# Optimization experiments

Measured on AMD Instinct MI355X. Metric: run time of the kernel, lower is better.

## Reference

```python
import jax, jax.numpy as jnp
import numpy as np

DECAY = 0.99
EPS = 1e-05
B, T, DIM, N_EMBED = 64, 1024, 256, 1024


def setup_inputs() -> dict:
    key = jax.random.key(0)
    k1, k2 = jax.random.split(key, 2)
    input_ = jax.random.normal(k1, (B, T, DIM), dtype=jnp.float32)
    embed = jax.random.normal(k2, (DIM, N_EMBED), dtype=jnp.float32)  # buffer 'embed'
    cluster_size = jnp.zeros((N_EMBED,), dtype=jnp.float32)           # buffer 'cluster_size'
    embed_avg = embed.copy()                                          # buffer 'embed_avg'
    return {"input_": input_, "embed": embed, "cluster_size": cluster_size, "embed_avg": embed_avg}


def reference(input_, embed, cluster_size, embed_avg):
    n_embed = embed.shape[1]
    flatten = input_.reshape(-1, embed.shape[0])  # [N, dim]
    dist = (jnp.sum(flatten * flatten, axis=-1, keepdims=True)
            - 2.0 * flatten @ embed
            + jnp.sum(embed * embed, axis=0, keepdims=True))
    embed_ind = jnp.argmin(dist, axis=1)  # (-dist).max(1) == argmin(dist)
    quantize = jnp.take(embed.T, embed_ind, axis=0).reshape(input_.shape)

    # training-mode EMA codebook update (buffers are detached in torch)
    # embed_onehot_sum = onehot.sum(0); embed_sum = flatten.T @ onehot
    # implemented via segment_sum (same math, no NxK one-hot materialized)
    ones = jnp.ones((flatten.shape[0],), dtype=flatten.dtype)
    embed_onehot_sum = jax.ops.segment_sum(ones, embed_ind, num_segments=n_embed)
    embed_sum = jax.ops.segment_sum(flatten, embed_ind, num_segments=n_embed).T  # [dim, n_embed]

    new_cluster_size = cluster_size * DECAY + (1.0 - DECAY) * embed_onehot_sum
    # NOTE: original code applies .mul_(decay) TWICE to embed_avg -> decay**2 (faithful)
    new_embed_avg = embed_avg * (DECAY * DECAY) + (1.0 - DECAY) * embed_sum
    n = jnp.sum(new_cluster_size)
    cs = (new_cluster_size + EPS) / (n + n_embed * EPS) * n
    new_embed = new_embed_avg / cs[None, :]

    diff = jnp.mean((jax.lax.stop_gradient(quantize) - input_) ** 2)
    quantize_st = input_ + jax.lax.stop_gradient(quantize - input_)
    return quantize_st, diff, embed_ind, new_cluster_size, new_embed_avg, new_embed
```

## Files before the change

kernel.cpp:

```cpp
#include <hip/hip_runtime.h>
#include <float.h>

#define DECAY 0.99f
#define EPS 1e-5f
#define NROWS 65536
#define DIM 256
#define NEMB 1024
#define CH 64
#define MAXSUB 2048

#define GLOBAL_AS __attribute__((address_space(1)))
#define LOCAL_AS  __attribute__((address_space(3)))

typedef _Float16 f16;
typedef _Float16 half8 __attribute__((ext_vector_type(8)));
typedef float f32x4 __attribute__((ext_vector_type(4)));

__global__ __launch_bounds__(256) void k_enorm(const float* __restrict__ embed,
                                               float* __restrict__ enorm2,
                                               int* __restrict__ counts) {
    int kk = threadIdx.x & 63;
    int dg = threadIdx.x >> 6;
    int k  = blockIdx.x * 64 + kk;
    float s = 0.f;
    for (int d = dg; d < DIM; d += 4) {
        float v = embed[(size_t)d * NEMB + k];
        s = fmaf(v, v, s);
    }
    __shared__ float red[4][64];
    red[dg][kk] = s;
    __syncthreads();
    if (dg == 0) enorm2[k] = red[0][kk] + red[1][kk] + red[2][kk] + red[3][kk];
    int gt = blockIdx.x * 256 + threadIdx.x;
    if (gt < NEMB) counts[gt] = 0;
}

__global__ __launch_bounds__(256) void k_prep(const float* __restrict__ embed,
                                              float* __restrict__ embedT,
                                              f16* __restrict__ ehlT) {
    __shared__ float tile[32][33];
    int c0 = blockIdx.x * 32, d0 = blockIdx.y * 32;
    int tx = threadIdx.x, ty = threadIdx.y;
#pragma unroll
    for (int i = 0; i < 4; i++)
        tile[ty + 8 * i][tx] = embed[(size_t)(d0 + ty + 8 * i) * NEMB + c0 + tx];
    __syncthreads();
#pragma unroll
    for (int i = 0; i < 4; i++) {
        int c = c0 + ty + 8 * i;
        int d = d0 + tx;
        float v = tile[tx][ty + 8 * i];
        embedT[(size_t)c * DIM + d] = v;
        f16 h = (f16)v;
        ehlT[(size_t)c * 512 + d]       = h;
        ehlT[(size_t)c * 512 + 256 + d] = (f16)(v - (float)h);
    }
}

#define LDS_A  0
#define LDS_B0 131072
#define LDS_B1 147456
#define LDS_SZ 163840

__global__ __launch_bounds__(512, 2) void k_argmin_mfma(const float* __restrict__ input,
                                                        const f16* __restrict__ ehlT,
                                                        const float* __restrict__ enorm2,
                                                        int* __restrict__ ind,
                                                        float* __restrict__ out_ind,
                                                        int* __restrict__ counts) {
    __shared__ char lds[LDS_SZ];
    const int tid  = threadIdx.x;
    const int lane = tid & 63;
    const int w    = tid >> 6;
    const int wr   = w >> 2;
    const int wc   = w & 3;
    const int rb   = blockIdx.x * 128;
    const int l15  = lane & 15;
    const int lkh  = lane >> 4;
    const int swa  = (l15 & 7) << 4;
    const int swb  = ((l15 >> 1) & 3) << 4;
    const int slot_log   = (lane & 3) ^ ((lane >> 3) & 3);
    const int gl_laneoff = (lane >> 2) * 512 + slot_log * 8;

    float e2a[4][4];
#pragma unroll
    for (int s = 0; s < 4; ++s)
#pragma unroll
        for (int fc = 0; fc < 4; ++fc)
            e2a[s][fc] = enorm2[s * 256 + wc * 64 + fc * 16 + l15];

#pragma unroll
    for (int i = 0; i < 2; i++) {
        int chunkid = w * 2 + i;
        const f16* src = ehlT + (size_t)chunkid * 8192 + gl_laneoff;
        __builtin_amdgcn_global_load_lds((const GLOBAL_AS unsigned*)src,
            (LOCAL_AS unsigned*)(lds + LDS_B0 + chunkid * 1024), 16, 0, 0);
    }

#pragma unroll
    for (int it8 = 0; it8 < 4; it8++) {
        int task = tid + 512 * it8;
        int row = task >> 4, ch = task & 15;
        const float4* g = (const float4*)(input + (size_t)(rb + row) * DIM + ch * 16);
        float fv[16];
        *(float4*)(fv + 0)  = g[0];
        *(float4*)(fv + 4)  = g[1];
        *(float4*)(fv + 8)  = g[2];
        *(float4*)(fv + 12) = g[3];
        half8 hh[2], llv[2];
#pragma unroll
        for (int u = 0; u < 2; u++)
#pragma unroll
            for (int e = 0; e < 8; e++) {
                float x = fv[u * 8 + e];
                f16 h = (f16)x;
                hh[u][e]  = h;
                llv[u][e] = (f16)(x - (float)h);
            }
        int rbase = row * 1024;
        int sw = (row & 7) << 4;
        *(half8*)(lds + LDS_A + rbase + (((ch * 2    ) * 16) ^ sw)) = hh[0];
        *(half8*)(lds + LDS_A + rbase + (((ch * 2 + 1) * 16) ^ sw)) = hh[1];
        *(half8*)(lds + LDS_A + rbase + (((32 + ch * 2) * 16) ^ sw)) = llv[0];
        *(half8*)(lds + LDS_A + rbase + (((33 + ch * 2) * 16) ^ sw)) = llv[1];
    }
    __syncthreads();

    float bv[16];
    int   bi[16];
#pragma unroll
    for (int q = 0; q < 16; q++) { bv[q] = FLT_MAX; bi[q] = 0x7fffffff; }

    int p = 0;
    for (int ct = 0; ct < 4; ct++) {
        const int cb = ct * 256;
        f32x4 acc[4][4];
#pragma unroll
        for (int fr = 0; fr < 4; fr++)
#pragma unroll
            for (int fc = 0; fc < 4; fc++) acc[fr][fc] = (f32x4){0.f, 0.f, 0.f, 0.f};

        for (int kt = 0; kt < 24; kt++) {
            const int it = ct * 24 + kt;
            if (it < 95) {
                int itn = it + 1;
                int ct2 = itn / 24;
                int kt2 = itn - ct2 * 24;
                int seg2 = kt2 >> 3, kq2 = kt2 & 7;
                int koff2 = ((seg2 == 2) ? 256 : 0) + kq2 * 32;
                const f16* base = ehlT + (size_t)ct2 * 131072 + koff2 + gl_laneoff;
                char* dstb = lds + (p ? LDS_B0 : LDS_B1);
#pragma unroll
                for (int i = 0; i < 2; i++) {
                    int chunkid = w * 2 + i;
                    __builtin_amdgcn_global_load_lds(
                        (const GLOBAL_AS unsigned*)(base + (size_t)chunkid * 8192),
                        (LOCAL_AS unsigned*)(dstb + chunkid * 1024), 16, 0, 0);
                }
                asm volatile("s_waitcnt vmcnt(2)" ::: "memory");
            } else {
                asm volatile("s_waitcnt vmcnt(0)" ::: "memory");
            }
            __builtin_amdgcn_s_barrier();
            __builtin_amdgcn_sched_barrier(0);

            const int seg = kt >> 3, kq = kt & 7;
            const int jslot = ((seg == 1) ? 32 : 0) + kq * 4 + lkh;
            const char* Bb = lds + (p ? LDS_B1 : LDS_B0);
            half8 af[4], bf[4];
#pragma unroll
            for (int f = 0; f < 4; f++) {
                int row = wr * 64 + f * 16 + l15;
                af[f] = *(const half8*)(lds + LDS_A + row * 1024 + ((jslot * 16) ^ swa));
            }
#pragma unroll
            for (int f = 0; f < 4; f++) {
                int col = wc * 64 + f * 16 + l15;
                bf[f] = *(const half8*)(Bb + col * 64 + ((lkh * 16) ^ swb));
            }
            __builtin_amdgcn_s_setprio(1);
#pragma unroll
            for (int fr = 0; fr < 4; fr++)
#pragma unroll
                for (int fc = 0; fc < 4; fc++)
                    acc[fr][fc] = __builtin_amdgcn_mfma_f32_16x16x32_f16(
                        af[fr], bf[fc], acc[fr][fc], 0, 0, 0);
            __builtin_amdgcn_s_setprio(0);

            if (kt == 23) {
#pragma unroll
                for (int fc = 0; fc < 4; fc++) {
                    int col = cb + wc * 64 + fc * 16 + l15;
                    float e2 = e2a[ct][fc];
#pragma unroll
                    for (int fr = 0; fr < 4; fr++)
#pragma unroll
                        for (int r = 0; r < 4; r++) {
                            float s = fmaf(-2.f, acc[fr][fc][r], e2);
                            int q = fr * 4 + r;
                            if (s < bv[q]) { bv[q] = s; bi[q] = col; }
                        }
                }
            }
            __builtin_amdgcn_s_barrier();
            p ^= 1;
        }
    }

#pragma unroll
    for (int q = 0; q < 16; q++) {
        float v = bv[q]; int i = bi[q];
#pragma unroll
        for (int m = 1; m <= 8; m <<= 1) {
            float ov = __shfl_xor(v, m, 64);
            int   oi = __shfl_xor(i, m, 64);
            if (ov < v || (ov == v && oi < i)) { v = ov; i = oi; }
        }
        bv[q] = v; bi[q] = i;
    }
    float* PV = (float*)(lds + LDS_B0);
    int*   PI = (int*)(lds + LDS_B0 + 2048);
    if (l15 == 0) {
#pragma unroll
        for (int fr = 0; fr < 4; fr++)
#pragma unroll
            for (int r = 0; r < 4; r++) {
                int rrow = wr * 64 + fr * 16 + lkh * 4 + r;
                PV[rrow * 4 + wc] = bv[fr * 4 + r];
                PI[rrow * 4 + wc] = bi[fr * 4 + r];
            }
    }
    __syncthreads();
    if (tid < 128) {
        float best = FLT_MAX; int bidx = 0x7fffffff;
#pragma unroll
        for (int t = 0; t < 4; t++) {
            float v = PV[tid * 4 + t];
            int   i = PI[tid * 4 + t];
            if (v < best || (v == best && i < bidx)) { best = v; bidx = i; }
        }
        ind[rb + tid] = bidx;
        out_ind[rb + tid] = (float)bidx;
        atomicAdd(&counts[bidx], 1);
    }
}

__global__ __launch_bounds__(256) void k_quant(const float* __restrict__ input,
                                               const float* __restrict__ embedT,
                                               const int* __restrict__ ind,
                                               float* __restrict__ out_q,
                                               float* __restrict__ partials) {
    const int tid = threadIdx.x;
    const unsigned gid = blockIdx.x * 256 + tid;
    float s = 0.f;
#pragma unroll
    for (int j = 0; j < 8; j++) {
        size_t i4 = (size_t)gid + (size_t)j * 524288u;
        int row = (int)(i4 >> 6);
        int d4  = (int)(i4 & 63);
        float4 iv = *reinterpret_cast<const float4*>(input + i4 * 4);
        int k = ind[row];
        float4 qv = *reinterpret_cast<const float4*>(embedT + (size_t)k * DIM + d4 * 4);
        float dx = qv.x - iv.x, dy = qv.y - iv.y, dz = qv.z - iv.z, dw = qv.w - iv.w;
        float4 ov;
        ov.x = iv.x + dx; ov.y = iv.y + dy; ov.z = iv.z + dz; ov.w = iv.w + dw;
        *reinterpret_cast<float4*>(out_q + i4 * 4) = ov;
        s += dx * dx + dy * dy + dz * dz + dw * dw;
    }
    __shared__ float red[256];
    red[tid] = s;
    __syncthreads();
    for (int off = 128; off > 0; off >>= 1) {
        if (tid < off) red[tid] += red[tid + off];
        __syncthreads();
    }
    if (tid == 0) partials[blockIdx.x] = red[0];
}

__global__ __launch_bounds__(1024) void k_scan(const int* __restrict__ counts,
                                               const float* __restrict__ cluster_size,
                                               const float* __restrict__ qpartials,
                                               int* __restrict__ offsets,
                                               int* __restrict__ cursor,
                                               int* __restrict__ substart,
                                               float* __restrict__ out_ncs,
                                               float* __restrict__ cs,
                                               float* __restrict__ out_diff) {
    __shared__ int sh[NEMB];
    __shared__ float shf[NEMB];
    int tid = threadIdx.x;
    shf[tid] = qpartials[tid] + qpartials[tid + 1024];
    __syncthreads();
    for (int off = 512; off > 0; off >>= 1) {
        if (tid < off) shf[tid] += shf[tid + off];
        __syncthreads();
    }
    if (tid == 0) out_diff[0] = shf[0] / 16777216.0f;
    __syncthreads();
    int c = counts[tid];
    sh[tid] = c;
    __syncthreads();
    for (int off = 1; off < NEMB; off <<= 1) {
        int t = (tid >= off) ? sh[tid - off] : 0;
        __syncthreads();
        sh[tid] += t;
        __syncthreads();
    }
    int excl = sh[tid] - c;
    offsets[tid] = excl;
    cursor[tid]  = excl;
    int sc = (c + CH - 1) / CH;
    __syncthreads();
    sh[tid] = sc;
    __syncthreads();
    for (int off = 1; off < NEMB; off <<= 1) {
        int t = (tid >= off) ? sh[tid - off] : 0;
        __syncthreads();
        sh[tid] += t;
        __syncthreads();
    }
    substart[tid] = sh[tid] - sc;
    if (tid == NEMB - 1) substart[NEMB] = sh[tid];
    float ncs = cluster_size[tid] * DECAY + (1.f - DECAY) * (float)c;
    out_ncs[tid] = ncs;
    shf[tid] = ncs;
    __syncthreads();
    for (int off = 512; off > 0; off >>= 1) {
        if (tid < off) shf[tid] += shf[tid + off];
        __syncthreads();
    }
    float n = shf[0];
    cs[tid] = (ncs + EPS) / (n + NEMB * EPS) * n;
}

__global__ __launch_bounds__(256) void k_scatter(const int* __restrict__ ind,
                                                 int* __restrict__ cursor,
                                                 int* __restrict__ sorted) {
    int i = blockIdx.x * 256 + threadIdx.x;
    int k = ind[i];
    int pos = atomicAdd(&cursor[k], 1);
    sorted[pos] = i;
}

__global__ __launch_bounds__(256) void k_psum(const float* __restrict__ input,
                                              const int* __restrict__ sorted,
                                              const int* __restrict__ counts,
                                              const int* __restrict__ offsets,
                                              const int* __restrict__ substart,
                                              float* __restrict__ partial) {
    const int b = blockIdx.x;
    if (b >= substart[NEMB]) return;
    int lo = 0, hi = NEMB;
    while (hi - lo > 1) {
        int mid = (lo + hi) >> 1;
        if (substart[mid] <= b) lo = mid; else hi = mid;
    }
    const int k     = lo;
    const int chunk = b - substart[k];
    const int cnt   = counts[k];
    const int base  = offsets[k] + chunk * CH;
    const int lim   = min(CH, cnt - chunk * CH);
    const int d     = threadIdx.x;
    float s = 0.f;
    for (int i = 0; i < lim; i++) {
        int row = sorted[base + i];
        s += input[(size_t)row * DIM + d];
    }
    partial[(size_t)b * DIM + d] = s;
}

__global__ __launch_bounds__(256) void k_ema(const float* __restrict__ partial,
                                             const float* __restrict__ embed_avg,
                                             const int* __restrict__ substart,
                                             const float* __restrict__ cs,
                                             float* __restrict__ out_navg,
                                             float* __restrict__ out_nembed) {
    const int d = blockIdx.x;
    const int t = threadIdx.x;
#pragma unroll
    for (int i = 0; i < 4; i++) {
        int k = t + 256 * i;
        int s0 = substart[k], s1 = substart[k + 1];
        float s = 0.f;
        for (int sub = s0; sub < s1; sub++)
            s += partial[(size_t)sub * DIM + d];
        float navg = embed_avg[(size_t)d * NEMB + k] * (DECAY * DECAY) + (1.f - DECAY) * s;
        out_navg[(size_t)d * NEMB + k] = navg;
        out_nembed[(size_t)d * NEMB + k] = navg / cs[k];
    }
}

extern "C" void kernel_launch(void* const* d_in, const int* in_sizes, int n_in,
                              void* d_out, int out_size, void* d_ws, size_t ws_size,
                              hipStream_t stream) {
    const float* input        = (const float*)d_in[0];
    const float* embed        = (const float*)d_in[1];
    const float* cluster_size = (const float*)d_in[2];
    const float* embed_avg    = (const float*)d_in[3];

    float* out        = (float*)d_out;
    float* out_q      = out;
    float* out_diff   = out + 16777216;
    float* out_ind    = out + 16777217;
    float* out_ncs    = out + 16842753;
    float* out_navg   = out + 16843777;
    float* out_nembed = out + 17105921;

    char* ws = (char*)d_ws;
    size_t o = 0;
    int*   w_ind      = (int*)(ws + o);   o += (size_t)NROWS * 4;
    float* w_embedT   = (float*)(ws + o); o += (size_t)DIM * NEMB * 4;
    float* w_enorm    = (float*)(ws + o); o += NEMB * 4;
    int*   w_counts   = (int*)(ws + o);   o += NEMB * 4;
    int*   w_offsets  = (int*)(ws + o);   o += NEMB * 4;
    int*   w_cursor   = (int*)(ws + o);   o += NEMB * 4;
    float* w_cs       = (float*)(ws + o); o += NEMB * 4;
    float* w_partials = (float*)(ws + o); o += 2048 * 4;
    int*   w_sorted   = (int*)(ws + o);   o += (size_t)NROWS * 4;
    int*   w_substart = (int*)(ws + o);   o += (NEMB + 4) * 4;
    float* w_partial  = (float*)(ws + o); o += (size_t)MAXSUB * DIM * 4;
    f16*   w_ehlT     = (f16*)(ws + o);   o += (size_t)NEMB * 512 * 2;

    k_enorm<<<16, 256, 0, stream>>>(embed, w_enorm, w_counts);
    k_prep<<<dim3(32, 8), dim3(32, 8), 0, stream>>>(embed, w_embedT, w_ehlT);
    k_argmin_mfma<<<NROWS / 128, 512, 0, stream>>>(input, w_ehlT, w_enorm,
                                                   w_ind, out_ind, w_counts);
    k_quant<<<2048, 256, 0, stream>>>(input, w_embedT, w_ind, out_q, w_partials);
    k_scan<<<1, 1024, 0, stream>>>(w_counts, cluster_size, w_partials, w_offsets,
                                   w_cursor, w_substart, out_ncs, w_cs, out_diff);
    k_scatter<<<NROWS / 256, 256, 0, stream>>>(w_ind, w_cursor, w_sorted);
    k_psum<<<MAXSUB, 256, 0, stream>>>(input, w_sorted, w_counts, w_offsets,
                                       w_substart, w_partial);
    k_ema<<<DIM, 256, 0, stream>>>(w_partial, embed_avg, w_substart, w_cs,
                                   out_navg, out_nembed);
}
```

Before: 309.3 us.

## Use single-f16 MFMA argmin with top-2 margin check and fp32 fix-up pass

The argmin GEMM now uses only the f16 high part of input and codebook instead of the hi/lo split, which cuts the K dimension and the LDS footprint to a third. Each row also tracks its second-best distance. Rows whose top-2 gap is within a fixed window (1.6) are flagged, compacted into a list and recomputed exactly in fp32 by a new fix kernel, which also updates their counts. The block is reshaped to 256 threads and 64 rows. The explicit vmcnt wait before the barrier is replaced by __syncthreads. The cost depends on how many rows get flagged, since the fp32 fix path is scalar and uses only 64 blocks. Correctness relies on the window bounding the f16 rounding error.

```diff
diff --git a/kernel.cpp b/kernel.cpp
--- a/kernel.cpp
+++ b/kernel.cpp
@@ -8,6 +8,7 @@
 #define NEMB 1024
 #define CH 64
 #define MAXSUB 2048
+#define WND 1.6f
 
 #define GLOBAL_AS __attribute__((address_space(1)))
 #define LOCAL_AS  __attribute__((address_space(3)))
@@ -18,7 +19,8 @@
 
 __global__ __launch_bounds__(256) void k_enorm(const float* __restrict__ embed,
                                                float* __restrict__ enorm2,
-                                               int* __restrict__ counts) {
+                                               int* __restrict__ counts,
+                                               int* __restrict__ nflag) {
     int kk = threadIdx.x & 63;
     int dg = threadIdx.x >> 6;
     int k  = blockIdx.x * 64 + kk;
@@ -33,11 +35,12 @@
     if (dg == 0) enorm2[k] = red[0][kk] + red[1][kk] + red[2][kk] + red[3][kk];
     int gt = blockIdx.x * 256 + threadIdx.x;
     if (gt < NEMB) counts[gt] = 0;
+    if (blockIdx.x == 0 && threadIdx.x == 0) nflag[0] = 0;
 }
 
 __global__ __launch_bounds__(256) void k_prep(const float* __restrict__ embed,
                                               float* __restrict__ embedT,
-                                              f16* __restrict__ ehlT) {
+                                              f16* __restrict__ ehT) {
     __shared__ float tile[32][33];
     int c0 = blockIdx.x * 32, d0 = blockIdx.y * 32;
     int tx = threadIdx.x, ty = threadIdx.y;
@@ -51,55 +54,50 @@
         int d = d0 + tx;
         float v = tile[tx][ty + 8 * i];
         embedT[(size_t)c * DIM + d] = v;
-        f16 h = (f16)v;
-        ehlT[(size_t)c * 512 + d]       = h;
-        ehlT[(size_t)c * 512 + 256 + d] = (f16)(v - (float)h);
+        ehT[(size_t)c * 256 + d] = (f16)v;
     }
 }
 
 #define LDS_A  0
-#define LDS_B0 131072
-#define LDS_B1 147456
-#define LDS_SZ 163840
-
-__global__ __launch_bounds__(512, 2) void k_argmin_mfma(const float* __restrict__ input,
-                                                        const f16* __restrict__ ehlT,
+#define LDS_B0 32768
+#define LDS_B1 49152
+#define LDS_SZ 65536
+
+__global__ __launch_bounds__(256, 2) void k_argmin_mfma(const float* __restrict__ input,
+                                                        const f16* __restrict__ ehT,
                                                         const float* __restrict__ enorm2,
                                                         int* __restrict__ ind,
                                                         float* __restrict__ out_ind,
-                                                        int* __restrict__ counts) {
+                                                        int* __restrict__ counts,
+                                                        unsigned char* __restrict__ flags) {
     __shared__ char lds[LDS_SZ];
     const int tid  = threadIdx.x;
     const int lane = tid & 63;
     const int w    = tid >> 6;
-    const int wr   = w >> 2;
-    const int wc   = w & 3;
-    const int rb   = blockIdx.x * 128;
+    const int rb   = blockIdx.x * 64;
     const int l15  = lane & 15;
     const int lkh  = lane >> 4;
-    const int swa  = (l15 & 7) << 4;
-    const int swb  = ((l15 >> 1) & 3) << 4;
     const int slot_log   = (lane & 3) ^ ((lane >> 3) & 3);
-    const int gl_laneoff = (lane >> 2) * 512 + slot_log * 8;
+    const int gl_laneoff = (lane >> 2) * 256 + slot_log * 8;
 
     float e2a[4][4];
 #pragma unroll
     for (int s = 0; s < 4; ++s)
 #pragma unroll
         for (int fc = 0; fc < 4; ++fc)
-            e2a[s][fc] = enorm2[s * 256 + wc * 64 + fc * 16 + l15];
-
-#pragma unroll
-    for (int i = 0; i < 2; i++) {
-        int chunkid = w * 2 + i;
-        const f16* src = ehlT + (size_t)chunkid * 8192 + gl_laneoff;
+            e2a[s][fc] = enorm2[s * 256 + w * 64 + fc * 16 + l15];
+
+#pragma unroll
+    for (int i = 0; i < 4; i++) {
+        int chunk = w * 4 + i;
+        const f16* src = ehT + (size_t)chunk * 4096 + gl_laneoff;
         __builtin_amdgcn_global_load_lds((const GLOBAL_AS unsigned*)src,
-            (LOCAL_AS unsigned*)(lds + LDS_B0 + chunkid * 1024), 16, 0, 0);
-    }
-
-#pragma unroll
-    for (int it8 = 0; it8 < 4; it8++) {
-        int task = tid + 512 * it8;
+            (LOCAL_AS unsigned*)(lds + LDS_B0 + chunk * 1024), 16, 0, 0);
+    }
+
+#pragma unroll
+    for (int it4 = 0; it4 < 4; it4++) {
+        int task = tid + 256 * it4;
         int row = task >> 4, ch = task & 15;
         const float4* g = (const float4*)(input + (size_t)(rb + row) * DIM + ch * 16);
         float fv[16];
@@ -107,141 +105,203 @@
         *(float4*)(fv + 4)  = g[1];
         *(float4*)(fv + 8)  = g[2];
         *(float4*)(fv + 12) = g[3];
-        half8 hh[2], llv[2];
+        half8 hh[2];
 #pragma unroll
         for (int u = 0; u < 2; u++)
 #pragma unroll
-            for (int e = 0; e < 8; e++) {
-                float x = fv[u * 8 + e];
-                f16 h = (f16)x;
-                hh[u][e]  = h;
-                llv[u][e] = (f16)(x - (float)h);
-            }
-        int rbase = row * 1024;
+            for (int e = 0; e < 8; e++) hh[u][e] = (f16)fv[u * 8 + e];
+        int rbase = row * 512;
         int sw = (row & 7) << 4;
         *(half8*)(lds + LDS_A + rbase + (((ch * 2    ) * 16) ^ sw)) = hh[0];
         *(half8*)(lds + LDS_A + rbase + (((ch * 2 + 1) * 16) ^ sw)) = hh[1];
-        *(half8*)(lds + LDS_A + rbase + (((32 + ch * 2) * 16) ^ sw)) = llv[0];
-        *(half8*)(lds + LDS_A + rbase + (((33 + ch * 2) * 16) ^ sw)) = llv[1];
-    }
-    __syncthreads();
-
-    float bv[16];
+    }
+    __syncthreads();
+
+    float bv[16], b2[16];
     int   bi[16];
 #pragma unroll
-    for (int q = 0; q < 16; q++) { bv[q] = FLT_MAX; bi[q] = 0x7fffffff; }
-
+    for (int q = 0; q < 16; q++) { bv[q] = FLT_MAX; b2[q] = FLT_MAX; bi[q] = 0x7fffffff; }
+
+    f32x4 acc[4][4];
     int p = 0;
-    for (int ct = 0; ct < 4; ct++) {
-        const int cb = ct * 256;
-        f32x4 acc[4][4];
+    for (int it = 0; it < 32; ++it) {
+        const int ct = it >> 3, kt = it & 7;
+        if (kt == 0) {
+#pragma unroll
+            for (int fr = 0; fr < 4; fr++)
+#pragma unroll
+                for (int fc = 0; fc < 4; fc++) acc[fr][fc] = (f32x4){0.f, 0.f, 0.f, 0.f};
+        }
+        if (it < 31) {
+            int itn = it + 1;
+            int ct2 = itn >> 3, kt2 = itn & 7;
+            const f16* base = ehT + (size_t)ct2 * 65536 + kt2 * 32 + gl_laneoff;
+            char* dstb = lds + (p ? LDS_B0 : LDS_B1);
+#pragma unroll
+            for (int i = 0; i < 4; i++) {
+                int chunk = w * 4 + i;
+                __builtin_amdgcn_global_load_lds(
+                    (const GLOBAL_AS unsigned*)(base + (size_t)chunk * 4096),
+                    (LOCAL_AS unsigned*)(dstb + chunk * 1024), 16, 0, 0);
+            }
+        }
+        const char* Bb = lds + (p ? LDS_B1 : LDS_B0);
+        half8 af[4], bf[4];
+#pragma unroll
+        for (int f = 0; f < 4; f++) {
+            int row = f * 16 + l15;
+            af[f] = *(const half8*)(lds + LDS_A + row * 512 +
+                                    (((kt * 4 + lkh) * 16) ^ ((row & 7) << 4)));
+        }
+#pragma unroll
+        for (int f = 0; f < 4; f++) {
+            int col = w * 64 + f * 16 + l15;
+            bf[f] = *(const half8*)(Bb + col * 64 + ((lkh * 16) ^ (((col >> 1) & 3) << 4)));
+        }
+        __builtin_amdgcn_s_setprio(1);
 #pragma unroll
         for (int fr = 0; fr < 4; fr++)
 #pragma unroll
-            for (int fc = 0; fc < 4; fc++) acc[fr][fc] = (f32x4){0.f, 0.f, 0.f, 0.f};
-
-        for (int kt = 0; kt < 24; kt++) {
-            const int it = ct * 24 + kt;
-            if (it < 95) {
-                int itn = it + 1;
-                int ct2 = itn / 24;
-                int kt2 = itn - ct2 * 24;
-                int seg2 = kt2 >> 3, kq2 = kt2 & 7;
-                int koff2 = ((seg2 == 2) ? 256 : 0) + kq2 * 32;
-                const f16* base = ehlT + (size_t)ct2 * 131072 + koff2 + gl_laneoff;
-                char* dstb = lds + (p ? LDS_B0 : LDS_B1);
-#pragma unroll
-                for (int i = 0; i < 2; i++) {
-                    int chunkid = w * 2 + i;
-                    __builtin_amdgcn_global_load_lds(
-                        (const GLOBAL_AS unsigned*)(base + (size_t)chunkid * 8192),
-                        (LOCAL_AS unsigned*)(dstb + chunkid * 1024), 16, 0, 0);
+            for (int fc = 0; fc < 4; fc++)
+                acc[fr][fc] = __builtin_amdgcn_mfma_f32_16x16x32_f16(
+                    af[fr], bf[fc], acc[fr][fc], 0, 0, 0);
+        __builtin_amdgcn_s_setprio(0);
+        if (kt == 7) {
+#pragma unroll
+            for (int fc = 0; fc < 4; fc++) {
+                int col = ct * 256 + w * 64 + fc * 16 + l15;
+                float e2 = e2a[ct][fc];
+#pragma unroll
+                for (int fr = 0; fr < 4; fr++)
+#pragma unroll
+                    for (int r = 0; r < 4; r++) {
+                        float s = fmaf(-2.f, acc[fr][fc][r], e2);
+                        int q = fr * 4 + r;
+                        if (s < bv[q]) { b2[q] = bv[q]; bv[q] = s; bi[q] = col; }
+                        else if (s < b2[q]) b2[q] = s;
+                    }
+            }
+        }
+        __syncthreads();
+        p ^= 1;
+    }
+
+#pragma unroll
+    for (int q = 0; q < 16; q++) {
+        float v1 = bv[q], v2 = b2[q]; int i1 = bi[q];
+#pragma unroll
+        for (int m = 1; m <= 8; m <<= 1) {
+            float ov1 = __shfl_xor(v1, m, 64);
+            int   oi1 = __shfl_xor(i1, m, 64);
+            float ov2 = __shfl_xor(v2, m, 64);
+            if (ov1 < v1 || (ov1 == v1 && oi1 < i1)) {
+                v2 = fminf(v1, ov2); v1 = ov1; i1 = oi1;
+            } else {
+                v2 = fminf(v2, ov1);
+            }
+        }
+        bv[q] = v1; bi[q] = i1; b2[q] = v2;
+    }
+    float* PV = (float*)(lds + LDS_B0);
+    int*   PI = (int*)(lds + LDS_B0 + 1024);
+    float* P2 = (float*)(lds + LDS_B0 + 2048);
+    if (l15 == 0) {
+#pragma unroll
+        for (int fr = 0; fr < 4; fr++)
+#pragma unroll
+            for (int r = 0; r < 4; r++) {
+                int rrow = fr * 16 + lkh * 4 + r;
+                PV[rrow * 4 + w] = bv[fr * 4 + r];
+                PI[rrow * 4 + w] = bi[fr * 4 + r];
+                P2[rrow * 4 + w] = b2[fr * 4 + r];
+            }
+    }
+    __syncthreads();
+    if (tid < 64) {
+        float v1 = PV[tid * 4]; int i1 = PI[tid * 4]; float v2 = P2[tid * 4];
+#pragma unroll
+        for (int t = 1; t < 4; t++) {
+            float ov1 = PV[tid * 4 + t]; int oi1 = PI[tid * 4 + t]; float ov2 = P2[tid * 4 + t];
+            if (ov1 < v1 || (ov1 == v1 && oi1 < i1)) {
+                v2 = fminf(v1, ov2); v1 = ov1; i1 = oi1;
+            } else {
+                v2 = fminf(v2, ov1);
+            }
+        }
+        int fl = (v2 - v1 <= WND) ? 1 : 0;
+        ind[rb + tid] = i1;
+        out_ind[rb + tid] = (float)i1;
+        flags[rb + tid] = (unsigned char)fl;
+        if (!fl) atomicAdd(&counts[i1], 1);
+    }
+}
+
+__global__ __launch_bounds__(256) void k_compact(const unsigned char* __restrict__ flags,
+                                                 int* __restrict__ nflag,
+                                                 int* __restrict__ flaglist) {
+    int i = blockIdx.x * 256 + threadIdx.x;
+    if (flags[i]) { int p = atomicAdd(nflag, 1); flaglist[p] = i; }
+}
+
+__global__ __launch_bounds__(256) void k_fix(const float* __restrict__ input,
+                                             const float* __restrict__ embed,
+                                             const float* __restrict__ enorm2,
+                                             const int* __restrict__ flaglist,
+                                             const int* __restrict__ nflag,
+                                             int* __restrict__ ind,
+                                             float* __restrict__ out_ind,
+                                             int* __restrict__ counts) {
+    __shared__ float xs[8][256];
+    __shared__ float rv[256];
+    __shared__ int   ri[256];
+    const int t = threadIdx.x;
+    const int total = nflag[0];
+    for (int base = blockIdx.x * 8; base < total; base += 64 * 8) {
+        const int nr = min(8, total - base);
+        __syncthreads();
+        for (int j = 0; j < nr; j++) {
+            int row = flaglist[base + j];
+            xs[j][t] = input[(size_t)row * DIM + t];
+        }
+        __syncthreads();
+        float best[8]; int bidx[8];
+#pragma unroll
+        for (int j = 0; j < 8; j++) { best[j] = FLT_MAX; bidx[j] = 0x7fffffff; }
+        for (int cc = 0; cc < 4; cc++) {
+            int c = cc * 256 + t;
+            float s[8];
+#pragma unroll
+            for (int j = 0; j < 8; j++) s[j] = 0.f;
+            for (int d = 0; d < 256; d++) {
+                float e = embed[(size_t)d * NEMB + c];
+#pragma unroll
+                for (int j = 0; j < 8; j++) s[j] = fmaf(xs[j][d], e, s[j]);
+            }
+            float e2 = enorm2[c];
+#pragma unroll
+            for (int j = 0; j < 8; j++) {
+                float dist = fmaf(-2.f, s[j], e2);
+                if (dist < best[j]) { best[j] = dist; bidx[j] = c; }
+            }
+        }
+        for (int j = 0; j < nr; j++) {
+            rv[t] = best[j]; ri[t] = bidx[j];
+            __syncthreads();
+            for (int off = 128; off > 0; off >>= 1) {
+                if (t < off) {
+                    float v = rv[t + off]; int i2 = ri[t + off];
+                    if (v < rv[t] || (v == rv[t] && i2 < ri[t])) { rv[t] = v; ri[t] = i2; }
                 }
-                asm volatile("s_waitcnt vmcnt(2)" ::: "memory");
-            } else {
-                asm volatile("s_waitcnt vmcnt(0)" ::: "memory");
-            }
-            __builtin_amdgcn_s_barrier();
-            __builtin_amdgcn_sched_barrier(0);
-
-            const int seg = kt >> 3, kq = kt & 7;
-            const int jslot = ((seg == 1) ? 32 : 0) + kq * 4 + lkh;
-            const char* Bb = lds + (p ? LDS_B1 : LDS_B0);
-            half8 af[4], bf[4];
-#pragma unroll
-            for (int f = 0; f < 4; f++) {
-                int row = wr * 64 + f * 16 + l15;
-                af[f] = *(const half8*)(lds + LDS_A + row * 1024 + ((jslot * 16) ^ swa));
-            }
-#pragma unroll
-            for (int f = 0; f < 4; f++) {
-                int col = wc * 64 + f * 16 + l15;
-                bf[f] = *(const half8*)(Bb + col * 64 + ((lkh * 16) ^ swb));
-            }
-            __builtin_amdgcn_s_setprio(1);
-#pragma unroll
-            for (int fr = 0; fr < 4; fr++)
-#pragma unroll
-                for (int fc = 0; fc < 4; fc++)
-                    acc[fr][fc] = __builtin_amdgcn_mfma_f32_16x16x32_f16(
-                        af[fr], bf[fc], acc[fr][fc], 0, 0, 0);
-            __builtin_amdgcn_s_setprio(0);
-
-            if (kt == 23) {
-#pragma unroll
-                for (int fc = 0; fc < 4; fc++) {
-                    int col = cb + wc * 64 + fc * 16 + l15;
-                    float e2 = e2a[ct][fc];
-#pragma unroll
-                    for (int fr = 0; fr < 4; fr++)
-#pragma unroll
-                        for (int r = 0; r < 4; r++) {
-                            float s = fmaf(-2.f, acc[fr][fc][r], e2);
-                            int q = fr * 4 + r;
-                            if (s < bv[q]) { bv[q] = s; bi[q] = col; }
-                        }
-                }
-            }
-            __builtin_amdgcn_s_barrier();
-            p ^= 1;
-        }
-    }
-
-#pragma unroll
-    for (int q = 0; q < 16; q++) {
-        float v = bv[q]; int i = bi[q];
-#pragma unroll
-        for (int m = 1; m <= 8; m <<= 1) {
-            float ov = __shfl_xor(v, m, 64);
-            int   oi = __shfl_xor(i, m, 64);
-            if (ov < v || (ov == v && oi < i)) { v = ov; i = oi; }
-        }
-        bv[q] = v; bi[q] = i;
-    }
-    float* PV = (float*)(lds + LDS_B0);
-    int*   PI = (int*)(lds + LDS_B0 + 2048);
-    if (l15 == 0) {
-#pragma unroll
-        for (int fr = 0; fr < 4; fr++)
-#pragma unroll
-            for (int r = 0; r < 4; r++) {
-                int rrow = wr * 64 + fr * 16 + lkh * 4 + r;
-                PV[rrow * 4 + wc] = bv[fr * 4 + r];
-                PI[rrow * 4 + wc] = bi[fr * 4 + r];
-            }
-    }
-    __syncthreads();
-    if (tid < 128) {
-        float best = FLT_MAX; int bidx = 0x7fffffff;
-#pragma unroll
-        for (int t = 0; t < 4; t++) {
-            float v = PV[tid * 4 + t];
-            int   i = PI[tid * 4 + t];
-            if (v < best || (v == best && i < bidx)) { best = v; bidx = i; }
-        }
-        ind[rb + tid] = bidx;
-        out_ind[rb + tid] = (float)bidx;
-        atomicAdd(&counts[bidx], 1);
+                __syncthreads();
+            }
+            if (t == 0) {
+                int row = flaglist[base + j];
+                ind[row] = ri[0];
+                out_ind[row] = (float)ri[0];
+                atomicAdd(&counts[ri[0]], 1);
+            }
+            __syncthreads();
+        }
     }
 }
 
@@ -419,12 +479,18 @@
     int*   w_sorted   = (int*)(ws + o);   o += (size_t)NROWS * 4;
     int*   w_substart = (int*)(ws + o);   o += (NEMB + 4) * 4;
     float* w_partial  = (float*)(ws + o); o += (size_t)MAXSUB * DIM * 4;
-    f16*   w_ehlT     = (f16*)(ws + o);   o += (size_t)NEMB * 512 * 2;
-
-    k_enorm<<<16, 256, 0, stream>>>(embed, w_enorm, w_counts);
-    k_prep<<<dim3(32, 8), dim3(32, 8), 0, stream>>>(embed, w_embedT, w_ehlT);
-    k_argmin_mfma<<<NROWS / 128, 512, 0, stream>>>(input, w_ehlT, w_enorm,
-                                                   w_ind, out_ind, w_counts);
+    f16*   w_ehT      = (f16*)(ws + o);   o += (size_t)NEMB * 256 * 2;
+    unsigned char* w_flags = (unsigned char*)(ws + o); o += NROWS;
+    int*   w_flaglist = (int*)(ws + o);   o += (size_t)NROWS * 4;
+    int*   w_nflag    = (int*)(ws + o);   o += 16;
+
+    k_enorm<<<16, 256, 0, stream>>>(embed, w_enorm, w_counts, w_nflag);
+    k_prep<<<dim3(32, 8), dim3(32, 8), 0, stream>>>(embed, w_embedT, w_ehT);
+    k_argmin_mfma<<<NROWS / 64, 256, 0, stream>>>(input, w_ehT, w_enorm,
+                                                  w_ind, out_ind, w_counts, w_flags);
+    k_compact<<<NROWS / 256, 256, 0, stream>>>(w_flags, w_nflag, w_flaglist);
+    k_fix<<<64, 256, 0, stream>>>(input, embed, w_enorm, w_flaglist, w_nflag,
+                                  w_ind, out_ind, w_counts);
     k_quant<<<2048, 256, 0, stream>>>(input, w_embedT, w_ind, out_q, w_partials);
     k_scan<<<1, 1024, 0, stream>>>(w_counts, cluster_size, w_partials, w_offsets,
                                    w_cursor, w_substart, out_ncs, w_cs, out_diff);
```

After: 1.222 ms. 3.95x slower.
